# Performance work log

Hardware: AMD Instinct MI355X
Metric: run time of the kernel (lower is better)

Reference implementation:

```python
import jax, jax.numpy as jnp
import numpy as np

N_HEAD, N_KV_HEAD, N_EMBD, SEQ_LEN = 16, 4, 1024, 2048
HEAD_DIM = N_EMBD // N_HEAD  # 64
B = 2


def _rope(x, cos, sin):
    # x: [B, T, H, D]; cos/sin: [1, T, 1, D//2]
    d = x.shape[-1] // 2
    x1, x2 = x[..., :d], x[..., d:]
    return jnp.concatenate([x1 * cos + x2 * sin, -x1 * sin + x2 * cos], axis=-1)


def setup_inputs() -> dict:
    key = jax.random.key(0)
    ks = jax.random.split(key, 5)
    x = jax.random.normal(ks[0], (B, SEQ_LEN, N_EMBD), dtype=jnp.float32)
    # real RoPE tables (base 10000)
    half = HEAD_DIM // 2
    inv_freq = 1.0 / (10000.0 ** (jnp.arange(half, dtype=jnp.float32) / half))
    ang = jnp.arange(SEQ_LEN, dtype=jnp.float32)[:, None] * inv_freq[None, :]  # [T, half]
    cos = jnp.cos(ang)[None, :, None, :]  # [1, T, 1, half]
    sin = jnp.sin(ang)[None, :, None, :]
    s = 0.02
    Wq = s * jax.random.normal(ks[1], (N_EMBD, N_HEAD * HEAD_DIM), dtype=jnp.float32)
    Wk = s * jax.random.normal(ks[2], (N_EMBD, N_KV_HEAD * HEAD_DIM), dtype=jnp.float32)
    Wv = s * jax.random.normal(ks[3], (N_EMBD, N_KV_HEAD * HEAD_DIM), dtype=jnp.float32)
    Wo = s * jax.random.normal(ks[4], (N_EMBD, N_EMBD), dtype=jnp.float32)
    return {"x": x, "cos": cos, "sin": sin, "Wq": Wq, "Wk": Wk, "Wv": Wv, "Wo": Wo}


def reference(x, cos, sin, Wq, Wk, Wv, Wo):
    Bsz, T, C = x.shape
    H, Hkv, D = N_HEAD, N_KV_HEAD, HEAD_DIM
    q = (x @ Wq).reshape(Bsz, T, H, D)
    k = (x @ Wk).reshape(Bsz, T, Hkv, D)
    v = (x @ Wv).reshape(Bsz, T, Hkv, D)
    q = _rope(q, cos, sin)
    k = _rope(k, cos, sin)
    # GQA: repeat kv heads to match query heads
    rep = H // Hkv
    k = jnp.repeat(k, rep, axis=2)  # [B, T, H, D]
    v = jnp.repeat(v, rep, axis=2)
    scale = 1.0 / np.sqrt(D).astype(np.float32)
    att = jnp.einsum('bqhd,bkhd->bhqk', q, k) * scale  # [B, H, T, T]
    causal = jnp.tril(jnp.ones((T, T), dtype=bool))
    att = jnp.where(causal[None, None, :, :], att, -jnp.inf)
    att = jax.nn.softmax(att, axis=-1)
    y = jnp.einsum('bhqk,bkhd->bqhd', att, v).reshape(Bsz, T, C)
    return y @ Wo
```

## Files before the change

kernel.cpp:

```cpp
#include <hip/hip_runtime.h>
#include <hip/hip_bf16.h>


typedef __attribute__((ext_vector_type(8))) short s16x8;
typedef __attribute__((ext_vector_type(4))) float f32x4;
typedef __attribute__((ext_vector_type(4))) unsigned short u16x4;

#define LOG2E 1.44269504088896340736f

__device__ __forceinline__ float bf2f(unsigned short u) {
  unsigned int i = ((unsigned int)u) << 16;
  return __builtin_bit_cast(float, i);
}
__device__ __forceinline__ unsigned short f2bf(float f) {
  unsigned int i = __builtin_bit_cast(unsigned int, f);
  i += 0x7fffu + ((i >> 16) & 1u);
  return (unsigned short)(i >> 16);
}
__device__ __forceinline__ unsigned int cvtpk(float lo, float hi) {
  unsigned int r;
  asm("v_cvt_pk_bf16_f32 %0, %1, %2" : "=v"(r) : "v"(lo), "v"(hi));
  return r;
}

__device__ __forceinline__ void async16(const void* g, void* l) {
  __builtin_amdgcn_global_load_lds(
      (const __attribute__((address_space(1))) void*)g,
      (__attribute__((address_space(3))) void*)l, 16, 0, 0);
}


__global__ void conv_f32_to_bf16(const float* __restrict__ in,
                                 unsigned short* __restrict__ out, int n) {
  int i = (blockIdx.x * blockDim.x + threadIdx.x) * 4;
  if (i + 3 < n) {
    float4 v = *(const float4*)(in + i);
    u16x4 o = { f2bf(v.x), f2bf(v.y), f2bf(v.z), f2bf(v.w) };
    *(u16x4*)(out + i) = o;
  }
}

__global__ void transpose_conv4(const float* __restrict__ W0,
                                const float* __restrict__ W1,
                                const float* __restrict__ W2,
                                const float* __restrict__ W3,
                                unsigned short* __restrict__ D0,
                                unsigned short* __restrict__ D1,
                                unsigned short* __restrict__ D2,
                                unsigned short* __restrict__ D3) {
  __shared__ float tile[32][33];
  int z = blockIdx.z;
  const float* W = (z == 0) ? W0 : (z == 1) ? W1 : (z == 2) ? W2 : W3;
  unsigned short* Wt = (z == 0) ? D0 : (z == 1) ? D1 : (z == 2) ? D2 : D3;
  int N = (z == 1 || z == 2) ? 256 : 1024;
  const int K = 1024;
  int n0 = blockIdx.x * 32, k0 = blockIdx.y * 32;
  if (n0 >= N) return;
  int tx = threadIdx.x, ty = threadIdx.y;
  for (int i = ty; i < 32; i += 8)
    tile[i][tx] = W[(size_t)(k0 + i) * N + n0 + tx];
  __syncthreads();
  for (int i = ty; i < 32; i += 8)
    Wt[(size_t)(n0 + i) * K + k0 + tx] = f2bf(tile[tx][i]);
}

__global__ void rope_qk(unsigned short* __restrict__ QKV,
                        const float* __restrict__ cosb,
                        const float* __restrict__ sinb) {
  int idx = blockIdx.x * blockDim.x + threadIdx.x;
  int d = idx & 31;
  int hh = (idx >> 5) % 20;
  int row = idx / (32 * 20);
  int t = row & 2047;
  size_t base;
  float mul;
  if (hh < 16) { base = (size_t)row * 1536 + hh * 64 + d;   mul = 0.125f * LOG2E; }
  else         { base = (size_t)row * 1536 + 1024 + (hh - 16) * 64 + d; mul = 1.0f; }
  float x1 = bf2f(QKV[base]), x2 = bf2f(QKV[base + 32]);
  float c = cosb[t * 32 + d], s = sinb[t * 32 + d];
  QKV[base]      = f2bf((x1 * c + x2 * s) * mul);
  QKV[base + 32] = f2bf((-x1 * s + x2 * c) * mul);
}

__global__ __launch_bounds__(256) void gemm_bt(
    const unsigned short* __restrict__ A, const unsigned short* __restrict__ Bt,
    void* __restrict__ Cp, int M, int N, int K, int c_f32) {
  __shared__ unsigned short As[128 * 64];
  __shared__ unsigned short Bs[64 * 64];
  int tid = threadIdx.x;
  int w = tid >> 6, l = tid & 63, g = l >> 4, lr = l & 15;
  int wr = w >> 1, wc = w & 1;

  int nb = gridDim.x, bid = blockIdx.x;
  int wg = (bid & 7) * (nb >> 3) + (bid >> 3);
  int nx = N >> 6;
  int m0 = (wg / nx) * 128, n0 = (wg % nx) * 64;
  int sk = lr & 7;

  f32x4 acc[4][2] = {};

  for (int k0 = 0; k0 < K; k0 += 64) {
#pragma unroll
    for (int i = 0; i < 4; ++i) {
      int c = i * 256 + tid;
      int row = c >> 3, srcu = ((c & 7) ^ (row & 7)) * 8;
      async16(A + (size_t)(m0 + row) * K + k0 + srcu, (char*)As + c * 16);
    }
#pragma unroll
    for (int i = 0; i < 2; ++i) {
      int c = i * 256 + tid;
      int row = c >> 3, srcu = ((c & 7) ^ (row & 7)) * 8;
      async16(Bt + (size_t)(n0 + row) * K + k0 + srcu, (char*)Bs + c * 16);
    }
    __syncthreads();

    s16x8 af[2][4], bfr[2][2];
#pragma unroll
    for (int ks = 0; ks < 2; ++ks) {
#pragma unroll
      for (int m = 0; m < 4; ++m)
        af[ks][m] = *(const s16x8*)(As + (wr * 64 + m * 16 + lr) * 64 +
                                    ((ks * 4 + g) ^ sk) * 8);
#pragma unroll
      for (int n = 0; n < 2; ++n)
        bfr[ks][n] = *(const s16x8*)(Bs + (wc * 32 + n * 16 + lr) * 64 +
                                     ((ks * 4 + g) ^ sk) * 8);
    }
#pragma unroll
    for (int ks = 0; ks < 2; ++ks)
#pragma unroll
      for (int m = 0; m < 4; ++m)
#pragma unroll
        for (int n = 0; n < 2; ++n)
          acc[m][n] = __builtin_amdgcn_mfma_f32_16x16x32_bf16(
              af[ks][m], bfr[ks][n], acc[m][n], 0, 0, 0);
    __syncthreads();
  }

  if (c_f32) {
    float* C = (float*)Cp;
#pragma unroll
    for (int m = 0; m < 4; ++m)
#pragma unroll
      for (int n = 0; n < 2; ++n)
#pragma unroll
        for (int r = 0; r < 4; ++r)
          C[(size_t)(m0 + wr * 64 + m * 16 + g * 4 + r) * N +
            n0 + wc * 32 + n * 16 + lr] = acc[m][n][r];
  } else {
    unsigned short* C = (unsigned short*)Cp;
#pragma unroll
    for (int m = 0; m < 4; ++m)
#pragma unroll
      for (int n = 0; n < 2; ++n)
#pragma unroll
        for (int r = 0; r < 4; ++r)
          C[(size_t)(m0 + wr * 64 + m * 16 + g * 4 + r) * N +
            n0 + wc * 32 + n * 16 + lr] = f2bf(acc[m][n][r]);
  }
}

__global__ __launch_bounds__(256) void attn_fused(
    const unsigned short* __restrict__ QKV, unsigned short* __restrict__ Y) {
  __shared__ unsigned short Kt[2][64 * 64];
  __shared__ unsigned short Vt[2][64 * 64];
  __shared__ unsigned short Pb[4][16 * 64];

  const int T = 2048, CS = 1536;
  int tid = threadIdx.x;
  int w = tid >> 6, l = tid & 63, g = l >> 4, lr = l & 15;
  int n = blockIdx.x;
  int ip = n >> 5;
  int bh = n & 31, b = bh >> 4, h = bh & 15, kvh = h >> 2;
  int sx = lr & 7;

  const unsigned short* Qp = QKV + (size_t)b * T * CS + h * 64;
  const unsigned short* Kp = QKV + (size_t)b * T * CS + 1024 + kvh * 64;
  const unsigned short* Vp = QKV + (size_t)b * T * CS + 1280 + kvh * 64;
  unsigned short* Pw = Pb[w];

  int kvE = (tid & 31) * 2, dcV = ((tid >> 5) & 7) * 8;

  for (int pass = 0; pass < 2; ++pass) {
    int qt = pass == 0 ? (31 - ip) : ip;
    int qw = qt * 64 + w * 16;
    int q_mine = qw + lr;

    s16x8 qf[2];
#pragma unroll
    for (int ks = 0; ks < 2; ++ks)
      qf[ks] = *(const s16x8*)(Qp + (size_t)q_mine * CS + ks * 32 + g * 8);

    f32x4 o[4] = {};
    float mrun = -1e30f, lrun = 0.f;
    int ntiles = qt + 1;

#pragma unroll
    for (int i = 0; i < 2; ++i) {
      int c = i * 256 + tid;
      int row = c >> 3, srcc = ((c & 7) ^ (row & 7)) * 8;
      async16(Kp + (size_t)row * CS + srcc, (char*)(&Kt[0][0]) + c * 16);
    }
    {
      s16x8 vE = *(const s16x8*)(Vp + (size_t)kvE * CS + dcV);
      s16x8 vO = *(const s16x8*)(Vp + (size_t)(kvE + 1) * CS + dcV);
#pragma unroll
      for (int j = 0; j < 8; ++j) {
        unsigned int pk = (unsigned int)(unsigned short)vE[j] |
                          ((unsigned int)(unsigned short)vO[j] << 16);
        *(unsigned int*)(&Vt[0][0] + (dcV + j) * 64 + (kvE ^ (j * 8))) = pk;
      }
    }
    __syncthreads();

    int cur = 0;
    for (int it = 0; it < ntiles; ++it) {
      int kv0 = it * 64;
      bool hasnext = (it + 1 < ntiles);

      s16x8 vE, vO;
      if (hasnext) {
        int kvn = kv0 + 64;
#pragma unroll
        for (int i = 0; i < 2; ++i) {
          int c = i * 256 + tid;
          int row = c >> 3, srcc = ((c & 7) ^ (row & 7)) * 8;
          async16(Kp + (size_t)(kvn + row) * CS + srcc,
                  (char*)(&Kt[cur ^ 1][0]) + c * 16);
        }
        vE = *(const s16x8*)(Vp + (size_t)(kvn + kvE) * CS + dcV);
        vO = *(const s16x8*)(Vp + (size_t)(kvn + kvE + 1) * CS + dcV);
      }

      const unsigned short* Kc = &Kt[cur][0];
      const unsigned short* Vc = &Vt[cur][0];
      f32x4 s[4];
      __builtin_amdgcn_s_setprio(1);
#pragma unroll
      for (int nf = 0; nf < 4; ++nf) {
        f32x4 z = {};
#pragma unroll
        for (int ks = 0; ks < 2; ++ks) {
          s16x8 kf = *(const s16x8*)(Kc + (nf * 16 + lr) * 64 +
                                     ((ks * 4 + g) ^ sx) * 8);
          z = __builtin_amdgcn_mfma_f32_16x16x32_bf16(kf, qf[ks], z, 0, 0, 0);
        }
        s[nf] = z;
      }
      __builtin_amdgcn_s_setprio(0);

      if (it == ntiles - 1) {
#pragma unroll
        for (int nf = 0; nf < 4; ++nf)
#pragma unroll
          for (int r = 0; r < 4; ++r)
            if (kv0 + nf * 16 + g * 4 + r > q_mine) s[nf][r] = -1e30f;
      }

      float mt = s[0][0];
#pragma unroll
      for (int nf = 0; nf < 4; ++nf)
#pragma unroll
        for (int r = 0; r < 4; ++r) mt = fmaxf(mt, s[nf][r]);
      mt = fmaxf(mt, __shfl_xor(mt, 16, 64));
      mt = fmaxf(mt, __shfl_xor(mt, 32, 64));

      if (__any(mt > mrun + 11.5416f)) {
        float mnew = fmaxf(mrun, mt);
        float corr = exp2f(mrun - mnew);
        float psum = 0.f;
#pragma unroll
        for (int nf = 0; nf < 4; ++nf)
#pragma unroll
          for (int r = 0; r < 4; ++r) {
            float p = exp2f(s[nf][r] - mnew);
            s[nf][r] = p;
            psum += p;
          }
        psum += __shfl_xor(psum, 16, 64);
        psum += __shfl_xor(psum, 32, 64);
        lrun = lrun * corr + psum;
        mrun = mnew;
#pragma unroll
        for (int r = 0; r < 4; ++r) {
          float cr = __shfl(corr, g * 4 + r, 64);
#pragma unroll
          for (int d0 = 0; d0 < 4; ++d0) o[d0][r] *= cr;
        }
      } else {
        float psum = 0.f;
#pragma unroll
        for (int nf = 0; nf < 4; ++nf)
#pragma unroll
          for (int r = 0; r < 4; ++r) {
            float p = exp2f(s[nf][r] - mrun);
            s[nf][r] = p;
            psum += p;
          }
        psum += __shfl_xor(psum, 16, 64);
        psum += __shfl_xor(psum, 32, 64);
        lrun += psum;
      }

#pragma unroll
      for (int nf = 0; nf < 4; ++nf) {
        uint2 pv;
        pv.x = cvtpk(s[nf][0], s[nf][1]);
        pv.y = cvtpk(s[nf][2], s[nf][3]);
        *(uint2*)(Pw + lr * 64 + ((nf * 16 + g * 4) ^ (sx * 8))) = pv;
      }
      asm volatile("s_waitcnt lgkmcnt(0)" ::: "memory");
      __builtin_amdgcn_sched_barrier(0);

      s16x8 pf[2];
#pragma unroll
      for (int ks = 0; ks < 2; ++ks)
        pf[ks] = *(const s16x8*)(Pw + lr * 64 + ((ks * 4 + g) ^ sx) * 8);
      __builtin_amdgcn_s_setprio(1);
#pragma unroll
      for (int d0 = 0; d0 < 4; ++d0)
#pragma unroll
        for (int ks = 0; ks < 2; ++ks) {
          s16x8 vf = *(const s16x8*)(Vc + (d0 * 16 + lr) * 64 +
                                     ((ks * 4 + g) ^ sx) * 8);
          o[d0] = __builtin_amdgcn_mfma_f32_16x16x32_bf16(pf[ks], vf, o[d0], 0, 0, 0);
        }
      __builtin_amdgcn_s_setprio(0);

      if (hasnext) {
        unsigned short* Vn = &Vt[cur ^ 1][0];
#pragma unroll
        for (int j = 0; j < 8; ++j) {
          unsigned int pk = (unsigned int)(unsigned short)vE[j] |
                            ((unsigned int)(unsigned short)vO[j] << 16);
          *(unsigned int*)(Vn + (dcV + j) * 64 + (kvE ^ (j * 8))) = pk;
        }
      }
      __syncthreads();
      cur ^= 1;
    }

#pragma unroll
    for (int r = 0; r < 4; ++r) {
      float lv = __shfl(lrun, g * 4 + r, 64);
      float inv = 1.f / lv;
      size_t rowoff = (size_t)(b * T + qw + g * 4 + r) * 1024 + h * 64;
#pragma unroll
      for (int d0 = 0; d0 < 4; ++d0)
        Y[rowoff + d0 * 16 + lr] = f2bf(o[d0][r] * inv);
    }
  }
}


extern "C" void kernel_launch(void* const* d_in, const int* in_sizes, int n_in,
                              void* d_out, int out_size, void* d_ws, size_t ws_size,
                              hipStream_t stream) {
  const float* x    = (const float*)d_in[0];
  const float* cosb = (const float*)d_in[1];
  const float* sinb = (const float*)d_in[2];
  const float* Wq   = (const float*)d_in[3];
  const float* Wk   = (const float*)d_in[4];
  const float* Wv   = (const float*)d_in[5];
  const float* Wo   = (const float*)d_in[6];
  float* out = (float*)d_out;

  char* ob = (char*)d_out;
  char* ws = (char*)d_ws;
  const size_t MB = 1024 * 1024;
  unsigned short* QKVb  = (unsigned short*)(ob);
  unsigned short* xb    = (unsigned short*)(ws);
  unsigned short* Wqkvt = (unsigned short*)(ws + 8 * MB);
  unsigned short* Wot   = (unsigned short*)(ws + 11 * MB);
  unsigned short* Yb    = xb;

  conv_f32_to_bf16<<<4096, 256, 0, stream>>>(x, xb, 4096 * 1024);
  transpose_conv4<<<dim3(32, 32, 4), dim3(32, 8), 0, stream>>>(
      Wq, Wk, Wv, Wo,
      Wqkvt, Wqkvt + (size_t)1024 * 1024, Wqkvt + (size_t)1280 * 1024, Wot);

  gemm_bt<<<dim3(768), 256, 0, stream>>>(xb, Wqkvt, QKVb, 4096, 1536, 1024, 0);

  rope_qk<<<10240, 256, 0, stream>>>(QKVb, cosb, sinb);

  attn_fused<<<dim3(512), 256, 0, stream>>>(QKVb, Yb);

  gemm_bt<<<dim3(512), 256, 0, stream>>>(Yb, Wot, out, 4096, 1024, 1024, 1);
}
```

Before: 122.0 us.

## Process both causal query tiles in one KV sweep sharing K/V loads

The attention kernel used to run two sequential passes per block, one for query tile 31-j and one for tile j, each streaming its own K/V tiles. Now one loop over KV tiles serves both query tiles: the shorter tile B only does work while it <= qtB, and K/V tiles and LDS fragments are loaded once for both. This removes the duplicate K/V global loads, LDS staging and barriers for the overlapping prefix. It doubles the per-thread accumulators and needs a second P buffer, so register pressure rises, and per-block work now varies from 17 to 32 iterations. The block-to-tile mapping is also reordered to interleave heavy and light blocks.

```diff
diff --git a/kernel.cpp b/kernel.cpp
--- a/kernel.cpp
+++ b/kernel.cpp
@@ -164,128 +164,155 @@
     const unsigned short* __restrict__ QKV, unsigned short* __restrict__ Y) {
   __shared__ unsigned short Kt[2][64 * 64];
   __shared__ unsigned short Vt[2][64 * 64];
-  __shared__ unsigned short Pb[4][16 * 64];
+  __shared__ unsigned short Pb[4][2][16 * 64];
 
   const int T = 2048, CS = 1536;
   int tid = threadIdx.x;
   int w = tid >> 6, l = tid & 63, g = l >> 4, lr = l & 15;
   int n = blockIdx.x;
-  int ip = n >> 5;
-  int bh = n & 31, b = bh >> 4, h = bh & 15, kvh = h >> 2;
+  int j, bh;
+  if (n < 256) { j = n >> 5;            bh = n & 31; }
+  else         { j = 15 - ((n - 256) >> 5); bh = (n - 256) & 31; }
+  int qtA = 31 - j, qtB = j;
+  int b = bh >> 4, h = bh & 15, kvh = h >> 2;
   int sx = lr & 7;
 
   const unsigned short* Qp = QKV + (size_t)b * T * CS + h * 64;
   const unsigned short* Kp = QKV + (size_t)b * T * CS + 1024 + kvh * 64;
   const unsigned short* Vp = QKV + (size_t)b * T * CS + 1280 + kvh * 64;
-  unsigned short* Pw = Pb[w];
+  unsigned short* PwA = Pb[w][0];
+  unsigned short* PwB = Pb[w][1];
 
   int kvE = (tid & 31) * 2, dcV = ((tid >> 5) & 7) * 8;
 
-  for (int pass = 0; pass < 2; ++pass) {
-    int qt = pass == 0 ? (31 - ip) : ip;
-    int qw = qt * 64 + w * 16;
-    int q_mine = qw + lr;
-
-    s16x8 qf[2];
-#pragma unroll
-    for (int ks = 0; ks < 2; ++ks)
-      qf[ks] = *(const s16x8*)(Qp + (size_t)q_mine * CS + ks * 32 + g * 8);
-
-    f32x4 o[4] = {};
-    float mrun = -1e30f, lrun = 0.f;
-    int ntiles = qt + 1;
-
-#pragma unroll
-    for (int i = 0; i < 2; ++i) {
-      int c = i * 256 + tid;
-      int row = c >> 3, srcc = ((c & 7) ^ (row & 7)) * 8;
-      async16(Kp + (size_t)row * CS + srcc, (char*)(&Kt[0][0]) + c * 16);
-    }
-    {
-      s16x8 vE = *(const s16x8*)(Vp + (size_t)kvE * CS + dcV);
-      s16x8 vO = *(const s16x8*)(Vp + (size_t)(kvE + 1) * CS + dcV);
-#pragma unroll
-      for (int j = 0; j < 8; ++j) {
-        unsigned int pk = (unsigned int)(unsigned short)vE[j] |
-                          ((unsigned int)(unsigned short)vO[j] << 16);
-        *(unsigned int*)(&Vt[0][0] + (dcV + j) * 64 + (kvE ^ (j * 8))) = pk;
-      }
-    }
-    __syncthreads();
-
-    int cur = 0;
-    for (int it = 0; it < ntiles; ++it) {
-      int kv0 = it * 64;
-      bool hasnext = (it + 1 < ntiles);
-
-      s16x8 vE, vO;
-      if (hasnext) {
-        int kvn = kv0 + 64;
-#pragma unroll
-        for (int i = 0; i < 2; ++i) {
-          int c = i * 256 + tid;
-          int row = c >> 3, srcc = ((c & 7) ^ (row & 7)) * 8;
-          async16(Kp + (size_t)(kvn + row) * CS + srcc,
-                  (char*)(&Kt[cur ^ 1][0]) + c * 16);
-        }
-        vE = *(const s16x8*)(Vp + (size_t)(kvn + kvE) * CS + dcV);
-        vO = *(const s16x8*)(Vp + (size_t)(kvn + kvE + 1) * CS + dcV);
-      }
-
-      const unsigned short* Kc = &Kt[cur][0];
-      const unsigned short* Vc = &Vt[cur][0];
-      f32x4 s[4];
-      __builtin_amdgcn_s_setprio(1);
+  int qwA = qtA * 64 + w * 16, qA = qwA + lr;
+  int qwB = qtB * 64 + w * 16, qB = qwB + lr;
+
+  s16x8 qfA[2], qfB[2];
+#pragma unroll
+  for (int ks = 0; ks < 2; ++ks) {
+    qfA[ks] = *(const s16x8*)(Qp + (size_t)qA * CS + ks * 32 + g * 8);
+    qfB[ks] = *(const s16x8*)(Qp + (size_t)qB * CS + ks * 32 + g * 8);
+  }
+
+  f32x4 oA[4] = {}, oB[4] = {};
+  float mA = -1e30f, lA = 0.f, mB = -1e30f, lB = 0.f;
+  int ntiles = qtA + 1;
+
+#pragma unroll
+  for (int i = 0; i < 2; ++i) {
+    int c = i * 256 + tid;
+    int row = c >> 3, srcc = ((c & 7) ^ (row & 7)) * 8;
+    async16(Kp + (size_t)row * CS + srcc, (char*)(&Kt[0][0]) + c * 16);
+  }
+  {
+    s16x8 vE = *(const s16x8*)(Vp + (size_t)kvE * CS + dcV);
+    s16x8 vO = *(const s16x8*)(Vp + (size_t)(kvE + 1) * CS + dcV);
+#pragma unroll
+    for (int jj = 0; jj < 8; ++jj) {
+      unsigned int pk = (unsigned int)(unsigned short)vE[jj] |
+                        ((unsigned int)(unsigned short)vO[jj] << 16);
+      *(unsigned int*)(&Vt[0][0] + (dcV + jj) * 64 + (kvE ^ (jj * 8))) = pk;
+    }
+  }
+  __syncthreads();
+
+  int cur = 0;
+  for (int it = 0; it < ntiles; ++it) {
+    int kv0 = it * 64;
+    bool hasnext = (it + 1 < ntiles);
+    bool actB = (it <= qtB);
+
+    s16x8 vE, vO;
+    if (hasnext) {
+      int kvn = kv0 + 64;
+#pragma unroll
+      for (int i = 0; i < 2; ++i) {
+        int c = i * 256 + tid;
+        int row = c >> 3, srcc = ((c & 7) ^ (row & 7)) * 8;
+        async16(Kp + (size_t)(kvn + row) * CS + srcc,
+                (char*)(&Kt[cur ^ 1][0]) + c * 16);
+      }
+      vE = *(const s16x8*)(Vp + (size_t)(kvn + kvE) * CS + dcV);
+      vO = *(const s16x8*)(Vp + (size_t)(kvn + kvE + 1) * CS + dcV);
+    }
+
+    const unsigned short* Kc = &Kt[cur][0];
+    const unsigned short* Vc = &Vt[cur][0];
+    f32x4 sA[4], sB[4];
+    __builtin_amdgcn_s_setprio(1);
+    if (actB) {
 #pragma unroll
       for (int nf = 0; nf < 4; ++nf) {
-        f32x4 z = {};
+        f32x4 zA = {}, zB = {};
 #pragma unroll
         for (int ks = 0; ks < 2; ++ks) {
           s16x8 kf = *(const s16x8*)(Kc + (nf * 16 + lr) * 64 +
                                      ((ks * 4 + g) ^ sx) * 8);
-          z = __builtin_amdgcn_mfma_f32_16x16x32_bf16(kf, qf[ks], z, 0, 0, 0);
-        }
-        s[nf] = z;
-      }
-      __builtin_amdgcn_s_setprio(0);
-
-      if (it == ntiles - 1) {
-#pragma unroll
-        for (int nf = 0; nf < 4; ++nf)
-#pragma unroll
-          for (int r = 0; r < 4; ++r)
-            if (kv0 + nf * 16 + g * 4 + r > q_mine) s[nf][r] = -1e30f;
-      }
-
-      float mt = s[0][0];
+          zA = __builtin_amdgcn_mfma_f32_16x16x32_bf16(kf, qfA[ks], zA, 0, 0, 0);
+          zB = __builtin_amdgcn_mfma_f32_16x16x32_bf16(kf, qfB[ks], zB, 0, 0, 0);
+        }
+        sA[nf] = zA; sB[nf] = zB;
+      }
+    } else {
+#pragma unroll
+      for (int nf = 0; nf < 4; ++nf) {
+        f32x4 zA = {};
+#pragma unroll
+        for (int ks = 0; ks < 2; ++ks) {
+          s16x8 kf = *(const s16x8*)(Kc + (nf * 16 + lr) * 64 +
+                                     ((ks * 4 + g) ^ sx) * 8);
+          zA = __builtin_amdgcn_mfma_f32_16x16x32_bf16(kf, qfA[ks], zA, 0, 0, 0);
+        }
+        sA[nf] = zA;
+      }
+    }
+    __builtin_amdgcn_s_setprio(0);
+
+    if (it == qtA) {
 #pragma unroll
       for (int nf = 0; nf < 4; ++nf)
 #pragma unroll
-        for (int r = 0; r < 4; ++r) mt = fmaxf(mt, s[nf][r]);
+        for (int r = 0; r < 4; ++r)
+          if (kv0 + nf * 16 + g * 4 + r > qA) sA[nf][r] = -1e30f;
+    }
+    if (actB && it == qtB) {
+#pragma unroll
+      for (int nf = 0; nf < 4; ++nf)
+#pragma unroll
+        for (int r = 0; r < 4; ++r)
+          if (kv0 + nf * 16 + g * 4 + r > qB) sB[nf][r] = -1e30f;
+    }
+
+    {
+      float mt = sA[0][0];
+#pragma unroll
+      for (int nf = 0; nf < 4; ++nf)
+#pragma unroll
+        for (int r = 0; r < 4; ++r) mt = fmaxf(mt, sA[nf][r]);
       mt = fmaxf(mt, __shfl_xor(mt, 16, 64));
       mt = fmaxf(mt, __shfl_xor(mt, 32, 64));
-
-      if (__any(mt > mrun + 11.5416f)) {
-        float mnew = fmaxf(mrun, mt);
-        float corr = exp2f(mrun - mnew);
+      if (__any(mt > mA + 11.5416f)) {
+        float mnew = fmaxf(mA, mt);
+        float corr = exp2f(mA - mnew);
         float psum = 0.f;
 #pragma unroll
         for (int nf = 0; nf < 4; ++nf)
 #pragma unroll
           for (int r = 0; r < 4; ++r) {
-            float p = exp2f(s[nf][r] - mnew);
-            s[nf][r] = p;
+            float p = exp2f(sA[nf][r] - mnew);
+            sA[nf][r] = p;
             psum += p;
           }
         psum += __shfl_xor(psum, 16, 64);
         psum += __shfl_xor(psum, 32, 64);
-        lrun = lrun * corr + psum;
-        mrun = mnew;
+        lA = lA * corr + psum;
+        mA = mnew;
 #pragma unroll
         for (int r = 0; r < 4; ++r) {
           float cr = __shfl(corr, g * 4 + r, 64);
 #pragma unroll
-          for (int d0 = 0; d0 < 4; ++d0) o[d0][r] *= cr;
+          for (int d0 = 0; d0 < 4; ++d0) oA[d0][r] *= cr;
         }
       } else {
         float psum = 0.f;
@@ -293,62 +320,139 @@
         for (int nf = 0; nf < 4; ++nf)
 #pragma unroll
           for (int r = 0; r < 4; ++r) {
-            float p = exp2f(s[nf][r] - mrun);
-            s[nf][r] = p;
+            float p = exp2f(sA[nf][r] - mA);
+            sA[nf][r] = p;
             psum += p;
           }
         psum += __shfl_xor(psum, 16, 64);
         psum += __shfl_xor(psum, 32, 64);
-        lrun += psum;
-      }
-
+        lA += psum;
+      }
+    }
+    if (actB) {
+      float mt = sB[0][0];
+#pragma unroll
+      for (int nf = 0; nf < 4; ++nf)
+#pragma unroll
+        for (int r = 0; r < 4; ++r) mt = fmaxf(mt, sB[nf][r]);
+      mt = fmaxf(mt, __shfl_xor(mt, 16, 64));
+      mt = fmaxf(mt, __shfl_xor(mt, 32, 64));
+      if (__any(mt > mB + 11.5416f)) {
+        float mnew = fmaxf(mB, mt);
+        float corr = exp2f(mB - mnew);
+        float psum = 0.f;
+#pragma unroll
+        for (int nf = 0; nf < 4; ++nf)
+#pragma unroll
+          for (int r = 0; r < 4; ++r) {
+            float p = exp2f(sB[nf][r] - mnew);
+            sB[nf][r] = p;
+            psum += p;
+          }
+        psum += __shfl_xor(psum, 16, 64);
+        psum += __shfl_xor(psum, 32, 64);
+        lB = lB * corr + psum;
+        mB = mnew;
+#pragma unroll
+        for (int r = 0; r < 4; ++r) {
+          float cr = __shfl(corr, g * 4 + r, 64);
+#pragma unroll
+          for (int d0 = 0; d0 < 4; ++d0) oB[d0][r] *= cr;
+        }
+      } else {
+        float psum = 0.f;
+#pragma unroll
+        for (int nf = 0; nf < 4; ++nf)
+#pragma unroll
+          for (int r = 0; r < 4; ++r) {
+            float p = exp2f(sB[nf][r] - mB);
+            sB[nf][r] = p;
+            psum += p;
+          }
+        psum += __shfl_xor(psum, 16, 64);
+        psum += __shfl_xor(psum, 32, 64);
+        lB += psum;
+      }
+    }
+
+#pragma unroll
+    for (int nf = 0; nf < 4; ++nf) {
+      uint2 pv;
+      pv.x = cvtpk(sA[nf][0], sA[nf][1]);
+      pv.y = cvtpk(sA[nf][2], sA[nf][3]);
+      *(uint2*)(PwA + lr * 64 + ((nf * 16 + g * 4) ^ (sx * 8))) = pv;
+    }
+    if (actB) {
 #pragma unroll
       for (int nf = 0; nf < 4; ++nf) {
         uint2 pv;
-        pv.x = cvtpk(s[nf][0], s[nf][1]);
-        pv.y = cvtpk(s[nf][2], s[nf][3]);
-        *(uint2*)(Pw + lr * 64 + ((nf * 16 + g * 4) ^ (sx * 8))) = pv;
-      }
-      asm volatile("s_waitcnt lgkmcnt(0)" ::: "memory");
-      __builtin_amdgcn_sched_barrier(0);
-
-      s16x8 pf[2];
+        pv.x = cvtpk(sB[nf][0], sB[nf][1]);
+        pv.y = cvtpk(sB[nf][2], sB[nf][3]);
+        *(uint2*)(PwB + lr * 64 + ((nf * 16 + g * 4) ^ (sx * 8))) = pv;
+      }
+    }
+    asm volatile("s_waitcnt lgkmcnt(0)" ::: "memory");
+    __builtin_amdgcn_sched_barrier(0);
+
+    s16x8 pfA[2], pfB[2];
+#pragma unroll
+    for (int ks = 0; ks < 2; ++ks)
+      pfA[ks] = *(const s16x8*)(PwA + lr * 64 + ((ks * 4 + g) ^ sx) * 8);
+    if (actB) {
 #pragma unroll
       for (int ks = 0; ks < 2; ++ks)
-        pf[ks] = *(const s16x8*)(Pw + lr * 64 + ((ks * 4 + g) ^ sx) * 8);
-      __builtin_amdgcn_s_setprio(1);
+        pfB[ks] = *(const s16x8*)(PwB + lr * 64 + ((ks * 4 + g) ^ sx) * 8);
+    }
+    __builtin_amdgcn_s_setprio(1);
+    if (actB) {
 #pragma unroll
       for (int d0 = 0; d0 < 4; ++d0)
 #pragma unroll
         for (int ks = 0; ks < 2; ++ks) {
           s16x8 vf = *(const s16x8*)(Vc + (d0 * 16 + lr) * 64 +
                                      ((ks * 4 + g) ^ sx) * 8);
-          o[d0] = __builtin_amdgcn_mfma_f32_16x16x32_bf16(pf[ks], vf, o[d0], 0, 0, 0);
-        }
-      __builtin_amdgcn_s_setprio(0);
-
-      if (hasnext) {
-        unsigned short* Vn = &Vt[cur ^ 1][0];
-#pragma unroll
-        for (int j = 0; j < 8; ++j) {
-          unsigned int pk = (unsigned int)(unsigned short)vE[j] |
-                            ((unsigned int)(unsigned short)vO[j] << 16);
-          *(unsigned int*)(Vn + (dcV + j) * 64 + (kvE ^ (j * 8))) = pk;
-        }
-      }
-      __syncthreads();
-      cur ^= 1;
-    }
-
-#pragma unroll
-    for (int r = 0; r < 4; ++r) {
-      float lv = __shfl(lrun, g * 4 + r, 64);
-      float inv = 1.f / lv;
-      size_t rowoff = (size_t)(b * T + qw + g * 4 + r) * 1024 + h * 64;
+          oA[d0] = __builtin_amdgcn_mfma_f32_16x16x32_bf16(pfA[ks], vf, oA[d0], 0, 0, 0);
+          oB[d0] = __builtin_amdgcn_mfma_f32_16x16x32_bf16(pfB[ks], vf, oB[d0], 0, 0, 0);
+        }
+    } else {
 #pragma unroll
       for (int d0 = 0; d0 < 4; ++d0)
-        Y[rowoff + d0 * 16 + lr] = f2bf(o[d0][r] * inv);
-    }
+#pragma unroll
+        for (int ks = 0; ks < 2; ++ks) {
+          s16x8 vf = *(const s16x8*)(Vc + (d0 * 16 + lr) * 64 +
+                                     ((ks * 4 + g) ^ sx) * 8);
+          oA[d0] = __builtin_amdgcn_mfma_f32_16x16x32_bf16(pfA[ks], vf, oA[d0], 0, 0, 0);
+        }
+    }
+    __builtin_amdgcn_s_setprio(0);
+
+    if (hasnext) {
+      unsigned short* Vn = &Vt[cur ^ 1][0];
+#pragma unroll
+      for (int jj = 0; jj < 8; ++jj) {
+        unsigned int pk = (unsigned int)(unsigned short)vE[jj] |
+                          ((unsigned int)(unsigned short)vO[jj] << 16);
+        *(unsigned int*)(Vn + (dcV + jj) * 64 + (kvE ^ (jj * 8))) = pk;
+      }
+    }
+    __syncthreads();
+    cur ^= 1;
+  }
+
+#pragma unroll
+  for (int r = 0; r < 4; ++r) {
+    float lvA = __shfl(lA, g * 4 + r, 64);
+    float invA = 1.f / lvA;
+    size_t roA = (size_t)(b * T + qwA + g * 4 + r) * 1024 + h * 64;
+#pragma unroll
+    for (int d0 = 0; d0 < 4; ++d0)
+      Y[roA + d0 * 16 + lr] = f2bf(oA[d0][r] * invA);
+    float lvB = __shfl(lB, g * 4 + r, 64);
+    float invB = 1.f / lvB;
+    size_t roB = (size_t)(b * T + qwB + g * 4 + r) * 1024 + h * 64;
+#pragma unroll
+    for (int d0 = 0; d0 < 4; ++d0)
+      Y[roB + d0 * 16 + lr] = f2bf(oB[d0][r] * invB);
   }
 }
 
```

New measurement: 125.8 us. +3.1%, slower.

## Process paired causal query tiles concurrently in one 512-thread attention block

Applied to the files above, without the earlier changes.

Attention blocks become 512 threads with two 4-wave groups. Each group handles one of a paired long and short query tile (31-j and j) at the same time, sharing the K/V tiles streamed into LDS, instead of running the two tiles in two sequential passes. This lets both tiles reuse each K/V tile load and puts more waves on each block. The cost is that the short-tile group sits idle (gated by an active flag) while the long tile finishes its remaining iterations. The block index mapping is also reordered so the longest pairs are scheduled first.

```diff
diff --git a/kernel.cpp b/kernel.cpp
--- a/kernel.cpp
+++ b/kernel.cpp
@@ -160,18 +160,22 @@
   }
 }
 
-__global__ __launch_bounds__(256) void attn_fused(
+__global__ __launch_bounds__(512, 4) void attn_fused(
     const unsigned short* __restrict__ QKV, unsigned short* __restrict__ Y) {
   __shared__ unsigned short Kt[2][64 * 64];
   __shared__ unsigned short Vt[2][64 * 64];
-  __shared__ unsigned short Pb[4][16 * 64];
+  __shared__ unsigned short Pb[8][16 * 64];
 
   const int T = 2048, CS = 1536;
   int tid = threadIdx.x;
   int w = tid >> 6, l = tid & 63, g = l >> 4, lr = l & 15;
+  int gw = w >> 2, ws = w & 3;
   int n = blockIdx.x;
-  int ip = n >> 5;
-  int bh = n & 31, b = bh >> 4, h = bh & 15, kvh = h >> 2;
+  int j, bh;
+  if (n < 256) { j = n >> 5;                bh = n & 31; }
+  else         { j = 15 - ((n - 256) >> 5); bh = (n - 256) & 31; }
+  int qtA = 31 - j, qtB = j;
+  int b = bh >> 4, h = bh & 15, kvh = h >> 2;
   int sx = lr & 7;
 
   const unsigned short* Qp = QKV + (size_t)b * T * CS + h * 64;
@@ -179,59 +183,57 @@
   const unsigned short* Vp = QKV + (size_t)b * T * CS + 1280 + kvh * 64;
   unsigned short* Pw = Pb[w];
 
-  int kvE = (tid & 31) * 2, dcV = ((tid >> 5) & 7) * 8;
-
-  for (int pass = 0; pass < 2; ++pass) {
-    int qt = pass == 0 ? (31 - ip) : ip;
-    int qw = qt * 64 + w * 16;
-    int q_mine = qw + lr;
-
-    s16x8 qf[2];
-#pragma unroll
-    for (int ks = 0; ks < 2; ++ks)
-      qf[ks] = *(const s16x8*)(Qp + (size_t)q_mine * CS + ks * 32 + g * 8);
-
-    f32x4 o[4] = {};
-    float mrun = -1e30f, lrun = 0.f;
-    int ntiles = qt + 1;
-
-#pragma unroll
-    for (int i = 0; i < 2; ++i) {
-      int c = i * 256 + tid;
+  int kvE = (tid & 31) * 2, dcV = ((tid >> 5) & 15) * 4;
+
+  int qt = (gw == 0) ? qtA : qtB;
+  int qw = qt * 64 + ws * 16;
+  int q_mine = qw + lr;
+
+  s16x8 qf[2];
+#pragma unroll
+  for (int ks = 0; ks < 2; ++ks)
+    qf[ks] = *(const s16x8*)(Qp + (size_t)q_mine * CS + ks * 32 + g * 8);
+
+  f32x4 o[4] = {};
+  float mrun = -1e30f, lrun = 0.f;
+  int ntiles = qtA + 1;
+
+  {
+    int c = tid;
+    int row = c >> 3, srcc = ((c & 7) ^ (row & 7)) * 8;
+    async16(Kp + (size_t)row * CS + srcc, (char*)(&Kt[0][0]) + c * 16);
+  }
+  {
+    u16x4 vE = *(const u16x4*)(Vp + (size_t)kvE * CS + dcV);
+    u16x4 vO = *(const u16x4*)(Vp + (size_t)(kvE + 1) * CS + dcV);
+#pragma unroll
+    for (int j4 = 0; j4 < 4; ++j4) {
+      int d = dcV + j4;
+      unsigned int pk = (unsigned int)(unsigned short)vE[j4] |
+                        ((unsigned int)(unsigned short)vO[j4] << 16);
+      *(unsigned int*)(&Vt[0][0] + d * 64 + (kvE ^ ((d & 7) * 8))) = pk;
+    }
+  }
+  __syncthreads();
+
+  int cur = 0;
+  for (int it = 0; it < ntiles; ++it) {
+    int kv0 = it * 64;
+    bool hasnext = (it + 1 < ntiles);
+    bool act = (it <= qt);
+
+    u16x4 vE, vO;
+    if (hasnext) {
+      int kvn = kv0 + 64;
+      int c = tid;
       int row = c >> 3, srcc = ((c & 7) ^ (row & 7)) * 8;
-      async16(Kp + (size_t)row * CS + srcc, (char*)(&Kt[0][0]) + c * 16);
-    }
-    {
-      s16x8 vE = *(const s16x8*)(Vp + (size_t)kvE * CS + dcV);
-      s16x8 vO = *(const s16x8*)(Vp + (size_t)(kvE + 1) * CS + dcV);
-#pragma unroll
-      for (int j = 0; j < 8; ++j) {
-        unsigned int pk = (unsigned int)(unsigned short)vE[j] |
-                          ((unsigned int)(unsigned short)vO[j] << 16);
-        *(unsigned int*)(&Vt[0][0] + (dcV + j) * 64 + (kvE ^ (j * 8))) = pk;
-      }
-    }
-    __syncthreads();
-
-    int cur = 0;
-    for (int it = 0; it < ntiles; ++it) {
-      int kv0 = it * 64;
-      bool hasnext = (it + 1 < ntiles);
-
-      s16x8 vE, vO;
-      if (hasnext) {
-        int kvn = kv0 + 64;
-#pragma unroll
-        for (int i = 0; i < 2; ++i) {
-          int c = i * 256 + tid;
-          int row = c >> 3, srcc = ((c & 7) ^ (row & 7)) * 8;
-          async16(Kp + (size_t)(kvn + row) * CS + srcc,
-                  (char*)(&Kt[cur ^ 1][0]) + c * 16);
-        }
-        vE = *(const s16x8*)(Vp + (size_t)(kvn + kvE) * CS + dcV);
-        vO = *(const s16x8*)(Vp + (size_t)(kvn + kvE + 1) * CS + dcV);
-      }
-
+      async16(Kp + (size_t)(kvn + row) * CS + srcc,
+              (char*)(&Kt[cur ^ 1][0]) + c * 16);
+      vE = *(const u16x4*)(Vp + (size_t)(kvn + kvE) * CS + dcV);
+      vO = *(const u16x4*)(Vp + (size_t)(kvn + kvE + 1) * CS + dcV);
+    }
+
+    if (act) {
       const unsigned short* Kc = &Kt[cur][0];
       const unsigned short* Vc = &Vt[cur][0];
       f32x4 s[4];
@@ -249,7 +251,7 @@
       }
       __builtin_amdgcn_s_setprio(0);
 
-      if (it == ntiles - 1) {
+      if (it == qt) {
 #pragma unroll
         for (int nf = 0; nf < 4; ++nf)
 #pragma unroll
@@ -326,29 +328,30 @@
           o[d0] = __builtin_amdgcn_mfma_f32_16x16x32_bf16(pf[ks], vf, o[d0], 0, 0, 0);
         }
       __builtin_amdgcn_s_setprio(0);
-
-      if (hasnext) {
-        unsigned short* Vn = &Vt[cur ^ 1][0];
-#pragma unroll
-        for (int j = 0; j < 8; ++j) {
-          unsigned int pk = (unsigned int)(unsigned short)vE[j] |
-                            ((unsigned int)(unsigned short)vO[j] << 16);
-          *(unsigned int*)(Vn + (dcV + j) * 64 + (kvE ^ (j * 8))) = pk;
-        }
-      }
-      __syncthreads();
-      cur ^= 1;
-    }
-
-#pragma unroll
-    for (int r = 0; r < 4; ++r) {
-      float lv = __shfl(lrun, g * 4 + r, 64);
-      float inv = 1.f / lv;
-      size_t rowoff = (size_t)(b * T + qw + g * 4 + r) * 1024 + h * 64;
-#pragma unroll
-      for (int d0 = 0; d0 < 4; ++d0)
-        Y[rowoff + d0 * 16 + lr] = f2bf(o[d0][r] * inv);
-    }
+    }
+
+    if (hasnext) {
+      unsigned short* Vn = &Vt[cur ^ 1][0];
+#pragma unroll
+      for (int j4 = 0; j4 < 4; ++j4) {
+        int d = dcV + j4;
+        unsigned int pk = (unsigned int)(unsigned short)vE[j4] |
+                          ((unsigned int)(unsigned short)vO[j4] << 16);
+        *(unsigned int*)(Vn + d * 64 + (kvE ^ ((d & 7) * 8))) = pk;
+      }
+    }
+    __syncthreads();
+    cur ^= 1;
+  }
+
+#pragma unroll
+  for (int r = 0; r < 4; ++r) {
+    float lv = __shfl(lrun, g * 4 + r, 64);
+    float inv = 1.f / lv;
+    size_t rowoff = (size_t)(b * T + qw + g * 4 + r) * 1024 + h * 64;
+#pragma unroll
+    for (int d0 = 0; d0 < 4; ++d0)
+      Y[rowoff + d0 * 16 + lr] = f2bf(o[d0][r] * inv);
   }
 }
 
@@ -383,7 +386,7 @@
 
   rope_qk<<<10240, 256, 0, stream>>>(QKVb, cosb, sinb);
 
-  attn_fused<<<dim3(512), 256, 0, stream>>>(QKVb, Yb);
+  attn_fused<<<dim3(512), 512, 0, stream>>>(QKVb, Yb);
 
   gemm_bt<<<dim3(512), 256, 0, stream>>>(Yb, Wot, out, 4096, 1024, 1024, 1);
 }
```

Result: faster. 118.3 us (median of 3 runs) (-3.0%).
